# Optimization experiments

Hardware: AMD Instinct MI355X
Metric: run time of the kernel (lower is better)

The kernel has to match this reference:

```python
import jax, jax.numpy as jnp
import numpy as np
from jax import lax

B_SZ, L, D, N, R = 1, 4096, 768, 16, 48  # R = dt_rank = ceil(D/16)


def _soft_clamp(x, lo=1e-4, hi=10.0):
    center = (hi + lo) / 2.0
    half_range = (hi - lo) / 2.0
    return center + half_range * jnp.tanh((x - center) / half_range)


def setup_inputs() -> dict:
    key = jax.random.key(0)
    ks = jax.random.split(key, 6)
    x = jax.random.normal(ks[0], (B_SZ, L, D), jnp.float32)
    # A_log init: log(1..N) broadcast over D (HiPPO-style S4D-real init)
    A_log = jnp.log(jnp.broadcast_to(jnp.arange(1, N + 1, dtype=jnp.float32), (D, N)))
    D_param = jnp.ones((D,), jnp.float32)
    # lecun_normal kernels
    W_bc = jax.random.normal(ks[1], (D, 2 * N), jnp.float32) / np.sqrt(D).astype(np.float32)
    W_dt = jax.random.normal(ks[2], (D, R), jnp.float32) / np.sqrt(D).astype(np.float32)
    W_dtp = jax.random.normal(ks[3], (R, D), jnp.float32) / np.sqrt(R).astype(np.float32)
    # dt bias init: inverse-softplus of uniform(dt_min, dt_max)
    dt = jax.random.uniform(ks[4], (D,), jnp.float32, 0.001, 0.1)
    dt = jnp.clip(dt, 1e-4)
    b_dt = dt + jnp.log(-jnp.expm1(-dt))
    rms_scale = jnp.ones((D,), jnp.float32)  # RMSNorm learnable scale
    return {"x": x, "A_log": A_log, "D_param": D_param, "W_bc": W_bc,
            "W_dt": W_dt, "W_dtp": W_dtp, "b_dt": b_dt, "rms_scale": rms_scale}


def reference(x, A_log, D_param, W_bc, W_dt, W_dtp, b_dt, rms_scale):
    n = A_log.shape[1]
    A = -jnp.exp(A_log)                                   # (D, N)
    bc = x @ W_bc                                         # (B, L, 2N)
    B_sel, C_sel = bc[..., :n], bc[..., n:]               # (B, L, N) each
    # delta = softplus(dt_proj(x_dt)) -> RMSNorm -> soft_clamp  (tustin mode)
    delta = jax.nn.softplus((x @ W_dt) @ W_dtp + b_dt)    # (B, L, D)
    delta = delta * lax.rsqrt(jnp.mean(delta * delta, axis=-1, keepdims=True) + 1e-6) * rms_scale
    delta = _soft_clamp(delta, 1e-4, 10.0)
    # Bilinear (Tustin) discretization, all fp32 already
    dE = delta[..., None]                                 # (B, L, D, 1)
    half = 0.5 * dE * A                                   # (B, L, D, N)
    denom = 1.0 - half
    A_bar = (1.0 + half) / denom                          # (B, L, D, N)
    B_bar = jnp.sqrt(dE) * B_sel[:, :, None, :] / denom   # (B, L, D, N)
    # trapezoidal input averaging
    x_prev = jnp.concatenate([jnp.zeros_like(x[:, :1]), x[:, :-1]], axis=1)
    x_in = 0.5 * (x + x_prev)                             # (B, L, D)
    Bx = B_bar * x_in[..., None]                          # (B, L, D, N)

    def op(left, right):
        a_l, b_l = left
        a_r, b_r = right
        return (a_r * a_l, a_r * b_l + b_r)

    _, all_h = lax.associative_scan(op, (A_bar, Bx), axis=1)
    y = jnp.sum(C_sel[:, :, None, :] * all_h, axis=-1)    # (B, L, D)
    return y + D_param * x
```

## Files before the change

kernel.cpp:

```cpp
#include <hip/hip_runtime.h>
#include <math.h>

#define LSEQ 4096
#define DD 768
#define NST 16
#define RNK 48
#define TCH 32
#define NCH (LSEQ / TCH)
#define KSTEPS 24
#define NTILES 5
#define WFRAG_N (KSTEPS * NTILES * 64 * 8)

typedef __attribute__((ext_vector_type(8))) short bf16x8;
typedef __attribute__((ext_vector_type(4))) float f32x4;

__device__ __forceinline__ float softplus_f(float z) {
    return fmaxf(z, 0.0f) + log1pf(expf(-fabsf(z)));
}

__device__ __forceinline__ float soft_clamp_f(float v) {
    const float ctr = 5.00005f;
    const float hr  = 4.99995f;
    const float inv_hr = 1.0f / 4.99995f;
    return ctr + hr * tanhf((v - ctr) * inv_hr);
}

__device__ __forceinline__ float wave_sum(float v) {
    #pragma unroll
    for (int m = 32; m >= 1; m >>= 1) v += __shfl_xor(v, m, 64);
    return v;
}

__device__ __forceinline__ unsigned short rne_bf16(float v) {
    unsigned u = __float_as_uint(v);
    return (unsigned short)((u + 0x7FFFu + ((u >> 16) & 1u)) >> 16);
}

__global__ __launch_bounds__(256) void k_prep(
    const float* __restrict__ W_dt, const float* __restrict__ W_bc,
    unsigned short* __restrict__ wf_hi, unsigned short* __restrict__ wf_lo)
{
    int i = blockIdx.x * 256 + threadIdx.x;
    if (i >= WFRAG_N) return;
    int j  = i & 7;
    int l  = (i >> 3) & 63;
    int nk = i >> 9;
    int n  = nk % NTILES;
    int kk = nk / NTILES;
    int k   = kk * 32 + (l >> 4) * 8 + j;
    int col = n * 16 + (l & 15);
    float v = (col < RNK) ? W_dt[k * RNK + col] : W_bc[k * 32 + (col - RNK)];
    unsigned short h = rne_bf16(v);
    float hf = __uint_as_float((unsigned)h << 16);
    wf_hi[i] = h;
    wf_lo[i] = rne_bf16(v - hf);
}

__global__ __launch_bounds__(512) void k_proj_mfma(
    const float* __restrict__ x,
    const unsigned short* __restrict__ wf_hi,
    const unsigned short* __restrict__ wf_lo,
    const float* __restrict__ W_dtp, const float* __restrict__ b_dt,
    const float* __restrict__ rms_scale,
    float* __restrict__ delta_out, float* __restrict__ bc_out)
{
    __shared__ __align__(16) float smem[16 * 772];
    __shared__ __align__(16) float t_lds[16][RNK];
    __shared__ float red2[8][16];

    const int tid  = threadIdx.x;
    const int lane = tid & 63;
    const int wq   = tid >> 6;
    const int mt   = blockIdx.x;

    {
        const float4* xg = (const float4*)(x + (size_t)mt * 16 * DD);
        #pragma unroll 2
        for (int idx = tid; idx < 3072; idx += 512) {
            int r = idx / 192, c4 = idx - r * 192;
            *(float4*)&smem[r * 772 + c4 * 4] = xg[idx];
        }
    }
    __syncthreads();

    const int rloc = lane & 15;
    const int ko   = (lane >> 4) * 8;

    f32x4 acc[NTILES];
    #pragma unroll
    for (int n = 0; n < NTILES; ++n) acc[n] = (f32x4){0.f, 0.f, 0.f, 0.f};

    #pragma unroll
    for (int k3 = 0; k3 < 3; ++k3) {
        const int kk = wq * 3 + k3;
        const float* xp = &smem[rloc * 772 + kk * 32 + ko];
        float4 xa = *(const float4*)xp;
        float4 xb = *(const float4*)(xp + 4);
        float va[8] = {xa.x, xa.y, xa.z, xa.w, xb.x, xb.y, xb.z, xb.w};
        bf16x8 ah, al;
        #pragma unroll
        for (int j = 0; j < 8; ++j) {
            unsigned short h = rne_bf16(va[j]);
            float hf = __uint_as_float((unsigned)h << 16);
            ah[j] = (short)h;
            al[j] = (short)rne_bf16(va[j] - hf);
        }
        const int base = kk * (NTILES * 512) + lane * 8;
        #pragma unroll
        for (int n = 0; n < NTILES; ++n) {
            bf16x8 bh = *(const bf16x8*)(wf_hi + base + n * 512);
            bf16x8 bl = *(const bf16x8*)(wf_lo + base + n * 512);
            acc[n] = __builtin_amdgcn_mfma_f32_16x16x32_bf16(al, bh, acc[n], 0, 0, 0);
            acc[n] = __builtin_amdgcn_mfma_f32_16x16x32_bf16(ah, bl, acc[n], 0, 0, 0);
            acc[n] = __builtin_amdgcn_mfma_f32_16x16x32_bf16(ah, bh, acc[n], 0, 0, 0);
        }
    }
    __syncthreads();

    if (wq > 0) {
        float* red = smem + ((wq - 1) * 64 + lane) * 20;
        #pragma unroll
        for (int n = 0; n < NTILES; ++n)
            #pragma unroll
            for (int r = 0; r < 4; ++r) red[n * 4 + r] = acc[n][r];
    }
    __syncthreads();
    if (wq == 0) {
        #pragma unroll
        for (int w = 0; w < 7; ++w) {
            const float* red = smem + (w * 64 + lane) * 20;
            #pragma unroll
            for (int n = 0; n < NTILES; ++n)
                #pragma unroll
                for (int r = 0; r < 4; ++r) acc[n][r] += red[n * 4 + r];
        }
        const int r0 = (lane >> 4) * 4;
        const int cb = lane & 15;
        #pragma unroll
        for (int n = 0; n < 3; ++n)
            #pragma unroll
            for (int r = 0; r < 4; ++r)
                t_lds[r0 + r][n * 16 + cb] = acc[n][r];
        #pragma unroll
        for (int n = 3; n < 5; ++n)
            #pragma unroll
            for (int r = 0; r < 4; ++r)
                bc_out[(size_t)(mt * 16 + r0 + r) * 32 + (n - 3) * 16 + cb] = acc[n][r];
    }
    __syncthreads();

    const int d0 = tid;
    const int d1 = tid + 512;
    const bool has2 = (tid < 256);

    float z0[16], z1[16];
    {
        float bb0 = b_dt[d0];
        float bb1 = has2 ? b_dt[d1] : 0.f;
        #pragma unroll
        for (int li = 0; li < 16; ++li) { z0[li] = bb0; z1[li] = bb1; }
    }
    #pragma unroll 2
    for (int r4 = 0; r4 < RNK; r4 += 4) {
        float w00 = W_dtp[(r4 + 0) * DD + d0];
        float w01 = W_dtp[(r4 + 1) * DD + d0];
        float w02 = W_dtp[(r4 + 2) * DD + d0];
        float w03 = W_dtp[(r4 + 3) * DD + d0];
        float w10 = has2 ? W_dtp[(r4 + 0) * DD + d1] : 0.f;
        float w11 = has2 ? W_dtp[(r4 + 1) * DD + d1] : 0.f;
        float w12 = has2 ? W_dtp[(r4 + 2) * DD + d1] : 0.f;
        float w13 = has2 ? W_dtp[(r4 + 3) * DD + d1] : 0.f;
        #pragma unroll
        for (int li = 0; li < 16; ++li) {
            float4 t4 = *(const float4*)&t_lds[li][r4];
            z0[li] = fmaf(t4.x, w00, z0[li]);
            z0[li] = fmaf(t4.y, w01, z0[li]);
            z0[li] = fmaf(t4.z, w02, z0[li]);
            z0[li] = fmaf(t4.w, w03, z0[li]);
            z1[li] = fmaf(t4.x, w10, z1[li]);
            z1[li] = fmaf(t4.y, w11, z1[li]);
            z1[li] = fmaf(t4.z, w12, z1[li]);
            z1[li] = fmaf(t4.w, w13, z1[li]);
        }
    }
    #pragma unroll
    for (int li = 0; li < 16; ++li) {
        z0[li] = softplus_f(z0[li]);
        z1[li] = has2 ? softplus_f(z1[li]) : 0.f;
    }
    #pragma unroll
    for (int li = 0; li < 16; ++li) {
        float ss = wave_sum(z0[li] * z0[li] + z1[li] * z1[li]);
        if (lane == 0) red2[wq][li] = ss;
    }
    __syncthreads();
    {
        float rs0 = rms_scale[d0];
        float rs1 = has2 ? rms_scale[d1] : 0.f;
        #pragma unroll
        for (int li = 0; li < 16; ++li) {
            float tot = 0.f;
            #pragma unroll
            for (int k = 0; k < 8; ++k) tot += red2[k][li];
            float inv = rsqrtf(tot * (1.0f / DD) + 1e-6f);
            size_t rowoff = (size_t)(mt * 16 + li) * DD;
            delta_out[rowoff + d0] = soft_clamp_f(z0[li] * inv * rs0);
            if (has2)
                delta_out[rowoff + d1] = soft_clamp_f(z1[li] * inv * rs1);
        }
    }
}

__global__ __launch_bounds__(256, 8) void k_scan1(
    const float* __restrict__ x, const float* __restrict__ delta,
    const float* __restrict__ bc, const float* __restrict__ A_log,
    float* __restrict__ Pbuf, float* __restrict__ Hbuf)
{
    __shared__ __align__(16) float xs[(TCH + 1) * 64];
    __shared__ __align__(16) float sqv[TCH * 64];
    __shared__ __align__(16) float bs[TCH * 16];

    const int tid = threadIdx.x;
    const int db  = blockIdx.x * 64;
    const int c   = blockIdx.y;
    const int l0  = c * TCH;

    for (int i = tid; i < (TCH + 1) * 16; i += 256) {
        int r = i >> 4, f = i & 15;
        int l = l0 - 1 + r;
        float4 v = (l >= 0) ? *(const float4*)&x[(size_t)l * DD + db + f * 4]
                            : make_float4(0.f, 0.f, 0.f, 0.f);
        *(float4*)&xs[r * 64 + f * 4] = v;
    }
    for (int i = tid; i < TCH * 16; i += 256) {
        int r = i >> 4, f = i & 15;
        float4 v = *(const float4*)&delta[(size_t)(l0 + r) * DD + db + f * 4];
        v.x = sqrtf(v.x); v.y = sqrtf(v.y); v.z = sqrtf(v.z); v.w = sqrtf(v.w);
        *(float4*)&sqv[r * 64 + f * 4] = v;
    }
    if (tid < TCH * 4) {
        int r = tid >> 2, f = tid & 3;
        *(float4*)&bs[r * 16 + f * 4] =
            *(const float4*)&bc[(size_t)(l0 + r) * 32 + f * 4];
    }

    const int lane = tid & 63;
    const int w    = tid >> 6;
    const int q    = lane >> 4;
    const int dlo  = (lane & 15) + w * 16;
    const int d    = db + dlo;

    float An[4];
    {
        float4 a = *(const float4*)&A_log[d * NST + q * 4];
        An[0] = -expf(a.x); An[1] = -expf(a.y);
        An[2] = -expf(a.z); An[3] = -expf(a.w);
    }
    __syncthreads();

    float h[4]  = {0.f, 0.f, 0.f, 0.f};
    float Pp[4] = {1.f, 1.f, 1.f, 1.f};
    float xprev = xs[dlo];

    #pragma unroll 4
    for (int ll = 0; ll < TCH; ++ll) {
        float xv = xs[(ll + 1) * 64 + dlo];
        float sq = sqv[ll * 64 + dlo];
        float4 Bc = *(const float4*)&bs[ll * 16 + q * 4];

        float xin = 0.5f * (xv + xprev);
        xprev = xv;
        float c0 = 0.5f * sq * sq;
        float c1 = sq * xin;

        float dn0 = fmaf(-c0, An[0], 1.0f);
        float dn1 = fmaf(-c0, An[1], 1.0f);
        float dn2 = fmaf(-c0, An[2], 1.0f);
        float dn3 = fmaf(-c0, An[3], 1.0f);
        float m01 = dn0 * dn1, m23 = dn2 * dn3;
        float ip  = __builtin_amdgcn_rcpf(m01 * m23);
        float ip01 = ip * m23, ip23 = ip * m01;
        float iv0 = ip01 * dn1, iv1 = ip01 * dn0;
        float iv2 = ip23 * dn3, iv3 = ip23 * dn2;
        float t10 = 2.0f - dn0, t11 = 2.0f - dn1;
        float t12 = 2.0f - dn2, t13 = 2.0f - dn3;

        Pp[0] *= t10 * iv0;
        Pp[1] *= t11 * iv1;
        Pp[2] *= t12 * iv2;
        Pp[3] *= t13 * iv3;
        h[0] = fmaf(t10, h[0], c1 * Bc.x) * iv0;
        h[1] = fmaf(t11, h[1], c1 * Bc.y) * iv1;
        h[2] = fmaf(t12, h[2], c1 * Bc.z) * iv2;
        h[3] = fmaf(t13, h[3], c1 * Bc.w) * iv3;
    }
    #pragma unroll
    for (int n = 0; n < 4; ++n) {
        int idx = (c * NST + q * 4 + n) * DD + d;
        Pbuf[idx] = Pp[n];
        Hbuf[idx] = h[n];
    }
}

__global__ __launch_bounds__(64) void k_scan2(
    float* __restrict__ Pbuf, const float* __restrict__ Hbuf)
{
    const int s = blockIdx.x * 64 + threadIdx.x;
    const int d = s % DD;
    const int n = s / DD;
    const int stride = NST * DD;

    int idx = n * DD + d;
    int idx_pf = idx;
    float p[8], h[8];
    #pragma unroll
    for (int i = 0; i < 8; ++i) {
        p[i] = Pbuf[idx_pf];
        h[i] = Hbuf[idx_pf];
        idx_pf += stride;
    }

    float carry = 0.f;
    for (int g = 0; g < NCH / 8; ++g) {
        float pn[8], hn[8];
        if (g + 1 < NCH / 8) {
            #pragma unroll
            for (int i = 0; i < 8; ++i) {
                pn[i] = Pbuf[idx_pf];
                hn[i] = Hbuf[idx_pf];
                idx_pf += stride;
            }
        }
        #pragma unroll
        for (int i = 0; i < 8; ++i) {
            Pbuf[idx] = carry;
            carry = fmaf(p[i], carry, h[i]);
            idx += stride;
        }
        #pragma unroll
        for (int i = 0; i < 8; ++i) { p[i] = pn[i]; h[i] = hn[i]; }
    }
}

__global__ __launch_bounds__(256, 8) void k_scan3(
    const float* __restrict__ x, const float* __restrict__ delta,
    const float* __restrict__ bc, const float* __restrict__ A_log,
    const float* __restrict__ carryin, const float* __restrict__ D_param,
    float* __restrict__ out)
{
    __shared__ __align__(16) float xs[(TCH + 1) * 64];
    __shared__ __align__(16) float sqv[TCH * 64];
    __shared__ __align__(16) float bs[TCH * 32];

    const int tid = threadIdx.x;
    const int db  = blockIdx.x * 64;
    const int c   = blockIdx.y;
    const int l0  = c * TCH;

    for (int i = tid; i < (TCH + 1) * 16; i += 256) {
        int r = i >> 4, f = i & 15;
        int l = l0 - 1 + r;
        float4 v = (l >= 0) ? *(const float4*)&x[(size_t)l * DD + db + f * 4]
                            : make_float4(0.f, 0.f, 0.f, 0.f);
        *(float4*)&xs[r * 64 + f * 4] = v;
    }
    for (int i = tid; i < TCH * 16; i += 256) {
        int r = i >> 4, f = i & 15;
        float4 v = *(const float4*)&delta[(size_t)(l0 + r) * DD + db + f * 4];
        v.x = sqrtf(v.x); v.y = sqrtf(v.y); v.z = sqrtf(v.z); v.w = sqrtf(v.w);
        *(float4*)&sqv[r * 64 + f * 4] = v;
    }
    for (int i = tid; i < TCH * 8; i += 256) {
        int r = i >> 3, f = i & 7;
        *(float4*)&bs[r * 32 + f * 4] =
            *(const float4*)&bc[(size_t)(l0 + r) * 32 + f * 4];
    }

    const int lane = tid & 63;
    const int w    = tid >> 6;
    const int q    = lane >> 4;
    const int dlo  = (lane & 15) + w * 16;
    const int d    = db + dlo;

    float An[4];
    {
        float4 a = *(const float4*)&A_log[d * NST + q * 4];
        An[0] = -expf(a.x); An[1] = -expf(a.y);
        An[2] = -expf(a.z); An[3] = -expf(a.w);
    }
    float h[4];
    #pragma unroll
    for (int n = 0; n < 4; ++n)
        h[n] = carryin[(c * NST + q * 4 + n) * DD + d];
    const float Dp = D_param[d];

    __syncthreads();

    float xprev = xs[dlo];
    #pragma unroll 4
    for (int ll = 0; ll < TCH; ++ll) {
        float xv = xs[(ll + 1) * 64 + dlo];
        float sq = sqv[ll * 64 + dlo];
        float4 Bc = *(const float4*)&bs[ll * 32 + q * 4];
        float4 Cc = *(const float4*)&bs[ll * 32 + 16 + q * 4];

        float xin = 0.5f * (xv + xprev);
        xprev = xv;
        float c0 = 0.5f * sq * sq;
        float c1 = sq * xin;

        float dn0 = fmaf(-c0, An[0], 1.0f);
        float dn1 = fmaf(-c0, An[1], 1.0f);
        float dn2 = fmaf(-c0, An[2], 1.0f);
        float dn3 = fmaf(-c0, An[3], 1.0f);
        float m01 = dn0 * dn1, m23 = dn2 * dn3;
        float ip  = __builtin_amdgcn_rcpf(m01 * m23);
        float ip01 = ip * m23, ip23 = ip * m01;
        float iv0 = ip01 * dn1, iv1 = ip01 * dn0;
        float iv2 = ip23 * dn3, iv3 = ip23 * dn2;
        float t10 = 2.0f - dn0, t11 = 2.0f - dn1;
        float t12 = 2.0f - dn2, t13 = 2.0f - dn3;

        h[0] = fmaf(t10, h[0], c1 * Bc.x) * iv0;
        h[1] = fmaf(t11, h[1], c1 * Bc.y) * iv1;
        h[2] = fmaf(t12, h[2], c1 * Bc.z) * iv2;
        h[3] = fmaf(t13, h[3], c1 * Bc.w) * iv3;

        float y = h[0] * Cc.x;
        y = fmaf(h[1], Cc.y, y);
        y = fmaf(h[2], Cc.z, y);
        y = fmaf(h[3], Cc.w, y);

        y += __shfl_xor(y, 16, 64);
        y += __shfl_xor(y, 32, 64);
        if (q == 0)
            out[(size_t)(l0 + ll) * DD + d] = fmaf(Dp, xv, y);
    }
}

extern "C" void kernel_launch(void* const* d_in, const int* in_sizes, int n_in,
                              void* d_out, int out_size, void* d_ws, size_t ws_size,
                              hipStream_t stream) {
    const float* x         = (const float*)d_in[0];
    const float* A_log     = (const float*)d_in[1];
    const float* D_param   = (const float*)d_in[2];
    const float* W_bc      = (const float*)d_in[3];
    const float* W_dt      = (const float*)d_in[4];
    const float* W_dtp     = (const float*)d_in[5];
    const float* b_dt      = (const float*)d_in[6];
    const float* rms_scale = (const float*)d_in[7];
    float* out = (float*)d_out;

    float* ws    = (float*)d_ws;
    float* delta = ws;
    float* bcbuf = delta + (size_t)LSEQ * DD;
    float* Pbuf  = bcbuf + (size_t)LSEQ * 32;
    float* Hbuf  = Pbuf + (size_t)NCH * NST * DD;
    unsigned short* wf_hi = (unsigned short*)(Hbuf + (size_t)NCH * NST * DD);
    unsigned short* wf_lo = wf_hi + WFRAG_N;

    k_prep<<<(WFRAG_N + 255) / 256, 256, 0, stream>>>(W_dt, W_bc, wf_hi, wf_lo);
    k_proj_mfma<<<LSEQ / 16, 512, 0, stream>>>(x, wf_hi, wf_lo, W_dtp, b_dt,
                                               rms_scale, delta, bcbuf);
    k_scan1<<<dim3(DD / 64, NCH), 256, 0, stream>>>(x, delta, bcbuf, A_log,
                                                    Pbuf, Hbuf);
    k_scan2<<<(DD * NST) / 64, 64, 0, stream>>>(Pbuf, Hbuf);
    k_scan3<<<dim3(DD / 64, NCH), 256, 0, stream>>>(x, delta, bcbuf, A_log,
                                                    Pbuf, D_param, out);
}
```

Before: 89.86 us.

## Use split-bf16 MFMA for dt up-projection and fuse chunk-carry scan into scan1

The dt up-projection (rank 48 to 768) moves from scalar FMAs reading W_dtp from global memory to bf16 hi/lo split MFMA, using weight fragments prepacked by the prep kernel. Softplus results are staged in shared memory before the RMS reduction. The separate carry-scan kernel is removed: the last chunk block of each d-slice, detected through an atomic counter, runs the cross-chunk carry propagation itself. This saves a launch and speeds up the projection, but adds a memset, a serial tail inside scan1, and a small precision change from the 3-term bf16 split.

```diff
diff --git a/kernel.cpp b/kernel.cpp
--- a/kernel.cpp
+++ b/kernel.cpp
@@ -10,6 +10,7 @@
 #define KSTEPS 24
 #define NTILES 5
 #define WFRAG_N (KSTEPS * NTILES * 64 * 8)
+#define WDTP_N  (2 * RNK * 64 * 8)
 
 typedef __attribute__((ext_vector_type(8))) short bf16x8;
 typedef __attribute__((ext_vector_type(4))) float f32x4;
@@ -38,30 +39,48 @@
 
 __global__ __launch_bounds__(256) void k_prep(
     const float* __restrict__ W_dt, const float* __restrict__ W_bc,
-    unsigned short* __restrict__ wf_hi, unsigned short* __restrict__ wf_lo)
+    const float* __restrict__ W_dtp,
+    unsigned short* __restrict__ wf_hi, unsigned short* __restrict__ wf_lo,
+    unsigned short* __restrict__ wp_hi, unsigned short* __restrict__ wp_lo)
 {
     int i = blockIdx.x * 256 + threadIdx.x;
-    if (i >= WFRAG_N) return;
-    int j  = i & 7;
-    int l  = (i >> 3) & 63;
-    int nk = i >> 9;
-    int n  = nk % NTILES;
-    int kk = nk / NTILES;
-    int k   = kk * 32 + (l >> 4) * 8 + j;
-    int col = n * 16 + (l & 15);
-    float v = (col < RNK) ? W_dt[k * RNK + col] : W_bc[k * 32 + (col - RNK)];
-    unsigned short h = rne_bf16(v);
-    float hf = __uint_as_float((unsigned)h << 16);
-    wf_hi[i] = h;
-    wf_lo[i] = rne_bf16(v - hf);
+    if (i < WFRAG_N) {
+        int j  = i & 7;
+        int l  = (i >> 3) & 63;
+        int nk = i >> 9;
+        int n  = nk % NTILES;
+        int kk = nk / NTILES;
+        int k   = kk * 32 + (l >> 4) * 8 + j;
+        int col = n * 16 + (l & 15);
+        float v = (col < RNK) ? W_dt[k * RNK + col] : W_bc[k * 32 + (col - RNK)];
+        unsigned short h = rne_bf16(v);
+        float hf = __uint_as_float((unsigned)h << 16);
+        wf_hi[i] = h;
+        wf_lo[i] = rne_bf16(v - hf);
+    } else if (i < WFRAG_N + WDTP_N) {
+        int ii = i - WFRAG_N;
+        int j  = ii & 7;
+        int l  = (ii >> 3) & 63;
+        int nk = ii >> 9;
+        int n  = nk % RNK;
+        int ks = nk / RNK;
+        int k   = ks * 32 + (l >> 4) * 8 + j;
+        int col = n * 16 + (l & 15);
+        float v = (k < RNK) ? W_dtp[k * DD + col] : 0.f;
+        unsigned short h = rne_bf16(v);
+        float hf = __uint_as_float((unsigned)h << 16);
+        wp_hi[ii] = h;
+        wp_lo[ii] = rne_bf16(v - hf);
+    }
 }
 
 __global__ __launch_bounds__(512) void k_proj_mfma(
     const float* __restrict__ x,
     const unsigned short* __restrict__ wf_hi,
     const unsigned short* __restrict__ wf_lo,
-    const float* __restrict__ W_dtp, const float* __restrict__ b_dt,
-    const float* __restrict__ rms_scale,
+    const unsigned short* __restrict__ wp_hi,
+    const unsigned short* __restrict__ wp_lo,
+    const float* __restrict__ b_dt, const float* __restrict__ rms_scale,
     float* __restrict__ delta_out, float* __restrict__ bc_out)
 {
     __shared__ __align__(16) float smem[16 * 772];
@@ -149,52 +168,68 @@
     }
     __syncthreads();
 
+    bf16x8 tah[2], tal[2];
+    #pragma unroll
+    for (int ks = 0; ks < 2; ++ks) {
+        const int kbase = ks * 32 + ko;
+        float tv[8];
+        #pragma unroll
+        for (int j = 0; j < 8; ++j)
+            tv[j] = (kbase + j < RNK) ? t_lds[rloc][kbase + j] : 0.f;
+        #pragma unroll
+        for (int j = 0; j < 8; ++j) {
+            unsigned short h = rne_bf16(tv[j]);
+            float hf = __uint_as_float((unsigned)h << 16);
+            tah[ks][j] = (short)h;
+            tal[ks][j] = (short)rne_bf16(tv[j] - hf);
+        }
+    }
+
+    const int r0 = (lane >> 4) * 4;
+    #pragma unroll
+    for (int nn = 0; nn < 6; ++nn) {
+        const int n = wq * 6 + nn;
+        f32x4 z = (f32x4){0.f, 0.f, 0.f, 0.f};
+        {
+            const int b0 = n * 512 + lane * 8;
+            bf16x8 bh = *(const bf16x8*)(wp_hi + b0);
+            bf16x8 bl = *(const bf16x8*)(wp_lo + b0);
+            z = __builtin_amdgcn_mfma_f32_16x16x32_bf16(tal[0], bh, z, 0, 0, 0);
+            z = __builtin_amdgcn_mfma_f32_16x16x32_bf16(tah[0], bl, z, 0, 0, 0);
+            z = __builtin_amdgcn_mfma_f32_16x16x32_bf16(tah[0], bh, z, 0, 0, 0);
+        }
+        {
+            const int b1 = (RNK + n) * 512 + lane * 8;
+            bf16x8 bh = *(const bf16x8*)(wp_hi + b1);
+            bf16x8 bl = *(const bf16x8*)(wp_lo + b1);
+            z = __builtin_amdgcn_mfma_f32_16x16x32_bf16(tal[1], bh, z, 0, 0, 0);
+            z = __builtin_amdgcn_mfma_f32_16x16x32_bf16(tah[1], bl, z, 0, 0, 0);
+            z = __builtin_amdgcn_mfma_f32_16x16x32_bf16(tah[1], bh, z, 0, 0, 0);
+        }
+        const int col = n * 16 + (lane & 15);
+        const float bb = b_dt[col];
+        #pragma unroll
+        for (int r = 0; r < 4; ++r)
+            smem[(r0 + r) * 772 + col] = softplus_f(z[r] + bb);
+    }
+    __syncthreads();
+
     const int d0 = tid;
     const int d1 = tid + 512;
     const bool has2 = (tid < 256);
-
-    float z0[16], z1[16];
     {
-        float bb0 = b_dt[d0];
-        float bb1 = has2 ? b_dt[d1] : 0.f;
-        #pragma unroll
-        for (int li = 0; li < 16; ++li) { z0[li] = bb0; z1[li] = bb1; }
-    }
-    #pragma unroll 2
-    for (int r4 = 0; r4 < RNK; r4 += 4) {
-        float w00 = W_dtp[(r4 + 0) * DD + d0];
-        float w01 = W_dtp[(r4 + 1) * DD + d0];
-        float w02 = W_dtp[(r4 + 2) * DD + d0];
-        float w03 = W_dtp[(r4 + 3) * DD + d0];
-        float w10 = has2 ? W_dtp[(r4 + 0) * DD + d1] : 0.f;
-        float w11 = has2 ? W_dtp[(r4 + 1) * DD + d1] : 0.f;
-        float w12 = has2 ? W_dtp[(r4 + 2) * DD + d1] : 0.f;
-        float w13 = has2 ? W_dtp[(r4 + 3) * DD + d1] : 0.f;
+        float sp0[16], sp1[16];
         #pragma unroll
         for (int li = 0; li < 16; ++li) {
-            float4 t4 = *(const float4*)&t_lds[li][r4];
-            z0[li] = fmaf(t4.x, w00, z0[li]);
-            z0[li] = fmaf(t4.y, w01, z0[li]);
-            z0[li] = fmaf(t4.z, w02, z0[li]);
-            z0[li] = fmaf(t4.w, w03, z0[li]);
-            z1[li] = fmaf(t4.x, w10, z1[li]);
-            z1[li] = fmaf(t4.y, w11, z1[li]);
-            z1[li] = fmaf(t4.z, w12, z1[li]);
-            z1[li] = fmaf(t4.w, w13, z1[li]);
-        }
-    }
-    #pragma unroll
-    for (int li = 0; li < 16; ++li) {
-        z0[li] = softplus_f(z0[li]);
-        z1[li] = has2 ? softplus_f(z1[li]) : 0.f;
-    }
-    #pragma unroll
-    for (int li = 0; li < 16; ++li) {
-        float ss = wave_sum(z0[li] * z0[li] + z1[li] * z1[li]);
-        if (lane == 0) red2[wq][li] = ss;
-    }
-    __syncthreads();
-    {
+            sp0[li] = smem[li * 772 + d0];
+            sp1[li] = has2 ? smem[li * 772 + d1] : 0.f;
+        }
+        #pragma unroll
+        for (int li = 0; li < 16; ++li) {
+            float ss = wave_sum(sp0[li] * sp0[li] + sp1[li] * sp1[li]);
+            if (lane == 0) red2[wq][li] = ss;
+        }
+        __syncthreads();
         float rs0 = rms_scale[d0];
         float rs1 = has2 ? rms_scale[d1] : 0.f;
         #pragma unroll
@@ -204,24 +239,27 @@
             for (int k = 0; k < 8; ++k) tot += red2[k][li];
             float inv = rsqrtf(tot * (1.0f / DD) + 1e-6f);
             size_t rowoff = (size_t)(mt * 16 + li) * DD;
-            delta_out[rowoff + d0] = soft_clamp_f(z0[li] * inv * rs0);
+            delta_out[rowoff + d0] = soft_clamp_f(sp0[li] * inv * rs0);
             if (has2)
-                delta_out[rowoff + d1] = soft_clamp_f(z1[li] * inv * rs1);
-        }
-    }
-}
-
-__global__ __launch_bounds__(256, 8) void k_scan1(
+                delta_out[rowoff + d1] = soft_clamp_f(sp1[li] * inv * rs1);
+        }
+    }
+}
+
+__global__ __launch_bounds__(256, 8) void k_scan1s(
     const float* __restrict__ x, const float* __restrict__ delta,
     const float* __restrict__ bc, const float* __restrict__ A_log,
-    float* __restrict__ Pbuf, float* __restrict__ Hbuf)
+    float* __restrict__ Pbuf, float* __restrict__ Hbuf,
+    int* __restrict__ done_ctr)
 {
     __shared__ __align__(16) float xs[(TCH + 1) * 64];
     __shared__ __align__(16) float sqv[TCH * 64];
     __shared__ __align__(16) float bs[TCH * 16];
+    __shared__ int s_last;
 
     const int tid = threadIdx.x;
-    const int db  = blockIdx.x * 64;
+    const int ds  = blockIdx.x;
+    const int db  = ds * 64;
     const int c   = blockIdx.y;
     const int l0  = c * TCH;
 
@@ -300,45 +338,45 @@
         Pbuf[idx] = Pp[n];
         Hbuf[idx] = h[n];
     }
-}
-
-__global__ __launch_bounds__(64) void k_scan2(
-    float* __restrict__ Pbuf, const float* __restrict__ Hbuf)
-{
-    const int s = blockIdx.x * 64 + threadIdx.x;
-    const int d = s % DD;
-    const int n = s / DD;
-    const int stride = NST * DD;
-
-    int idx = n * DD + d;
-    int idx_pf = idx;
-    float p[8], h[8];
-    #pragma unroll
-    for (int i = 0; i < 8; ++i) {
-        p[i] = Pbuf[idx_pf];
-        h[i] = Hbuf[idx_pf];
-        idx_pf += stride;
-    }
-
-    float carry = 0.f;
-    for (int g = 0; g < NCH / 8; ++g) {
-        float pn[8], hn[8];
-        if (g + 1 < NCH / 8) {
-            #pragma unroll
-            for (int i = 0; i < 8; ++i) {
-                pn[i] = Pbuf[idx_pf];
-                hn[i] = Hbuf[idx_pf];
-                idx_pf += stride;
+
+    __threadfence();
+    __syncthreads();
+    if (tid == 0) {
+        int prev = __hip_atomic_fetch_add(&done_ctr[ds], 1,
+                                          __ATOMIC_ACQ_REL, __HIP_MEMORY_SCOPE_AGENT);
+        s_last = (prev == NCH - 1);
+    }
+    __syncthreads();
+    if (!s_last) return;
+
+    {
+        const int stride = NST * DD;
+        int bidx[4];
+        #pragma unroll
+        for (int i = 0; i < 4; ++i)
+            bidx[i] = (q * 4 + i) * DD + d;
+        float carry[4] = {0.f, 0.f, 0.f, 0.f};
+        for (int g = 0; g < NCH / 4; ++g) {
+            float p[4][4], hh[4][4];
+            #pragma unroll
+            for (int cc = 0; cc < 4; ++cc) {
+                int coff = (g * 4 + cc) * stride;
+                #pragma unroll
+                for (int i = 0; i < 4; ++i) {
+                    p[cc][i]  = Pbuf[bidx[i] + coff];
+                    hh[cc][i] = Hbuf[bidx[i] + coff];
+                }
             }
-        }
-        #pragma unroll
-        for (int i = 0; i < 8; ++i) {
-            Pbuf[idx] = carry;
-            carry = fmaf(p[i], carry, h[i]);
-            idx += stride;
-        }
-        #pragma unroll
-        for (int i = 0; i < 8; ++i) { p[i] = pn[i]; h[i] = hn[i]; }
+            #pragma unroll
+            for (int cc = 0; cc < 4; ++cc) {
+                int coff = (g * 4 + cc) * stride;
+                #pragma unroll
+                for (int i = 0; i < 4; ++i) {
+                    Pbuf[bidx[i] + coff] = carry[i];
+                    carry[i] = fmaf(p[cc][i], carry[i], hh[cc][i]);
+                }
+            }
+        }
     }
 }
 
@@ -458,13 +496,17 @@
     float* Hbuf  = Pbuf + (size_t)NCH * NST * DD;
     unsigned short* wf_hi = (unsigned short*)(Hbuf + (size_t)NCH * NST * DD);
     unsigned short* wf_lo = wf_hi + WFRAG_N;
-
-    k_prep<<<(WFRAG_N + 255) / 256, 256, 0, stream>>>(W_dt, W_bc, wf_hi, wf_lo);
-    k_proj_mfma<<<LSEQ / 16, 512, 0, stream>>>(x, wf_hi, wf_lo, W_dtp, b_dt,
-                                               rms_scale, delta, bcbuf);
-    k_scan1<<<dim3(DD / 64, NCH), 256, 0, stream>>>(x, delta, bcbuf, A_log,
-                                                    Pbuf, Hbuf);
-    k_scan2<<<(DD * NST) / 64, 64, 0, stream>>>(Pbuf, Hbuf);
+    unsigned short* wp_hi = wf_lo + WFRAG_N;
+    unsigned short* wp_lo = wp_hi + WDTP_N;
+    int* done_ctr = (int*)(wp_lo + WDTP_N);
+
+    hipMemsetAsync(done_ctr, 0, 12 * sizeof(int), stream);
+    k_prep<<<(WFRAG_N + WDTP_N + 255) / 256, 256, 0, stream>>>(
+        W_dt, W_bc, W_dtp, wf_hi, wf_lo, wp_hi, wp_lo);
+    k_proj_mfma<<<LSEQ / 16, 512, 0, stream>>>(x, wf_hi, wf_lo, wp_hi, wp_lo,
+                                               b_dt, rms_scale, delta, bcbuf);
+    k_scan1s<<<dim3(12, NCH), 256, 0, stream>>>(x, delta, bcbuf, A_log,
+                                                Pbuf, Hbuf, done_ctr);
     k_scan3<<<dim3(DD / 64, NCH), 256, 0, stream>>>(x, delta, bcbuf, A_log,
                                                     Pbuf, D_param, out);
 }
```

Result: slower. 307.1 us (+241.8%).
